# Kernel optimization log

Hardware: AMD Instinct MI355X
Metric: run time of the kernel (lower is better)

Reference implementation:

```python
import jax, jax.numpy as jnp
import numpy as np

N, IN_DIM, H, D = 4096, 512, 8, 64
NEG = -1e9  # additive mask value for non-edges


def setup_inputs() -> dict:
    key = jax.random.key(0)
    k1, k2, k3, k4, k5, k6 = jax.random.split(key, 6)
    data = jax.random.normal(k1, (N, IN_DIM), dtype=jnp.float32)
    r = jax.random.uniform(k2, (N, N), dtype=jnp.float32)
    connectivity = jnp.where(r < 0.05, 0.0, NEG).astype(jnp.float32)
    # xavier-uniform-ish init for params
    lim_w = float(np.sqrt(6.0 / (IN_DIM + H * D)))
    W = jax.random.uniform(k3, (H * D, IN_DIM), jnp.float32, -lim_w, lim_w)
    b = jnp.zeros((H * D,), jnp.float32)
    lim_p = float(np.sqrt(6.0 / (H * D + 1)))
    src_proj = jax.random.uniform(k4, (1, H, D), jnp.float32, -lim_p, lim_p)
    trg_proj = jax.random.uniform(k5, (1, H, D), jnp.float32, -lim_p, lim_p)
    return {"data": data, "connectivity": connectivity, "W": W, "b": b,
            "src_proj": src_proj, "trg_proj": trg_proj}


def reference(data, connectivity, W, b, src_proj, trg_proj):
    # dropout is identity in eval mode (reference is deterministic)
    data1 = (data @ W.T + b).reshape(N, H, D)          # (N,H,D)
    src = jnp.einsum('nhd,xhd->nh', data1, src_proj)   # (N,H)
    trg = jnp.einsum('nhd,xhd->nh', data1, trg_proj)   # (N,H)
    # scores: (H,N,1) + (H,1,N) broadcast outer-sum
    e = src.T[:, :, None] + trg.T[:, None, :]          # (H,N,N)
    e = jnp.where(e >= 0, e, 0.01 * e)                 # LeakyReLU(0.01)
    e = e + connectivity[None, :, :]                   # additive mask
    scores = jax.nn.softmax(e, axis=-1)                # (H,N,N)
    # bmm over heads: (H,N,N) x (H,N,D) -> (H,N,D)
    out = jnp.einsum('hnm,hmd->hnd', scores, data1.transpose(1, 0, 2))
    out = out.transpose(1, 0, 2).reshape(N, H * D)     # concat=True
    return out
```

## Files before the change

### kernel.cpp

```cpp
#include <hip/hip_runtime.h>
#include <hip/hip_bf16.h>

#define NN 4096
#define IN_DIM 512
#define NH 8
#define DD 64
#define HD 512
#define QCAP 128
#define RCAP 448


typedef __attribute__((ext_vector_type(8))) short short8;
typedef __attribute__((ext_vector_type(4))) float f32x4;
typedef __attribute__((ext_vector_type(2))) float f32x2;

static __device__ __forceinline__ unsigned short f2bf(float x) {
    __hip_bfloat16 h = __float2bfloat16(x);
    return *reinterpret_cast<unsigned short*>(&h);
}

__global__ __launch_bounds__(256) void k_cast2(const float* __restrict__ inA,
                                               unsigned short* __restrict__ outA,
                                               int n4A,
                                               const float* __restrict__ inB,
                                               unsigned short* __restrict__ outB,
                                               int n4B) {
    int t = blockIdx.x * 256 + threadIdx.x;
    const float* in;
    unsigned short* out;
    if (t < n4A) {
        in = inA; out = outA;
    } else {
        t -= n4A;
        if (t >= n4B) return;
        in = inB; out = outB;
    }
    float4 v = ((const float4*)in)[t];
    ushort4 o;
    o.x = f2bf(v.x); o.y = f2bf(v.y); o.z = f2bf(v.z); o.w = f2bf(v.w);
    ((ushort4*)out)[t] = o;
}

__global__ __launch_bounds__(256) void k_gemm_fused(const unsigned short* __restrict__ Ab,
                                                    const unsigned short* __restrict__ Wb,
                                                    const float* __restrict__ bias,
                                                    const float* __restrict__ sp,
                                                    const float* __restrict__ tp,
                                                    unsigned short* __restrict__ Cb,
                                                    float* __restrict__ src,
                                                    float* __restrict__ trg) {
    const int lane = threadIdx.x & 63;
    const int w = threadIdx.x >> 6;
    const int col = lane & 15;
    const int quad = lane >> 4;
    const int koff = quad * 8;
    const int h = blockIdx.x;
    const int m0 = h * 64;
    const int n0 = blockIdx.y * 64;

    const short8* ap  = (const short8*)(Ab + (size_t)(n0 + w * 16 + col) * IN_DIM + koff);
    const short8* bp0 = (const short8*)(Wb + (size_t)(m0 +  0 + col) * IN_DIM + koff);
    const short8* bp1 = (const short8*)(Wb + (size_t)(m0 + 16 + col) * IN_DIM + koff);
    const short8* bp2 = (const short8*)(Wb + (size_t)(m0 + 32 + col) * IN_DIM + koff);
    const short8* bp3 = (const short8*)(Wb + (size_t)(m0 + 48 + col) * IN_DIM + koff);

    f32x4 acc0 = {0.f, 0.f, 0.f, 0.f}, acc1 = acc0, acc2 = acc0, acc3 = acc0;

#pragma unroll 4
    for (int ks = 0; ks < 16; ks++) {
        short8 a  = ap[ks * 4];
        short8 b0 = bp0[ks * 4];
        short8 b1 = bp1[ks * 4];
        short8 b2 = bp2[ks * 4];
        short8 b3 = bp3[ks * 4];
        acc0 = __builtin_amdgcn_mfma_f32_16x16x32_bf16(a, b0, acc0, 0, 0, 0);
        acc1 = __builtin_amdgcn_mfma_f32_16x16x32_bf16(a, b1, acc1, 0, 0, 0);
        acc2 = __builtin_amdgcn_mfma_f32_16x16x32_bf16(a, b2, acc2, 0, 0, 0);
        acc3 = __builtin_amdgcn_mfma_f32_16x16x32_bf16(a, b3, acc3, 0, 0, 0);
    }

    const int rbase = n0 + w * 16 + quad * 4;
    f32x4 accs[4] = {acc0, acc1, acc2, acc3};
    float ps[4] = {0.f, 0.f, 0.f, 0.f};
    float pt[4] = {0.f, 0.f, 0.f, 0.f};
#pragma unroll
    for (int mt = 0; mt < 4; mt++) {
        const int m = m0 + mt * 16 + col;
        const float bv  = bias[m];
        const float spv = sp[m];
        const float tpv = tp[m];
#pragma unroll
        for (int r = 0; r < 4; r++) {
            float v = accs[mt][r] + bv;
            Cb[(size_t)(rbase + r) * HD + m] = f2bf(v);
            ps[r] += v * spv;
            pt[r] += v * tpv;
        }
    }
#pragma unroll
    for (int off = 1; off <= 8; off <<= 1) {
#pragma unroll
        for (int r = 0; r < 4; r++) {
            ps[r] += __shfl_xor(ps[r], off, 64);
            pt[r] += __shfl_xor(pt[r], off, 64);
        }
    }
    if (col < 4)
        src[(rbase + col) * 8 + h] = ps[col];
    else if (col < 8)
        trg[(rbase + col - 4) * 8 + h] = pt[col - 4];
}

__global__ __launch_bounds__(256) void k_rowattn(const float* __restrict__ conn,
                                                 const float* __restrict__ src,
                                                 const float* __restrict__ trg,
                                                 const unsigned short* __restrict__ d1b,
                                                 float* __restrict__ out) {
    __shared__ unsigned short seg[4][QCAP];
    __shared__ unsigned short elist[RCAP + 8];
    __shared__ int wcnt[4];
    __shared__ float cbuf[3][64][9];
    const int w = threadIdx.x >> 6, lane = threadIdx.x & 63;
    const int i = blockIdx.x;
    const int h = lane >> 3, d8 = lane & 7;

    const float* crow = conn + (size_t)i * NN + w * 1024;
    int cnt = 0;
#pragma unroll
    for (int c0 = 0; c0 < 1024; c0 += 256) {
        float4 c = *(const float4*)(crow + c0 + lane * 4);
        float cv[4] = {c.x, c.y, c.z, c.w};
#pragma unroll
        for (int q = 0; q < 4; q++) {
            bool edge = (cv[q] == 0.0f);
            unsigned long long mask = __ballot(edge);
            int pre = __popcll(mask & ((1ull << lane) - 1ull));
            int pos = cnt + pre;
            if (edge && pos < QCAP)
                seg[w][pos] = (unsigned short)(w * 1024 + c0 + lane * 4 + q);
            cnt += __popcll(mask);
        }
    }
    if (cnt > QCAP) cnt = QCAP;
    if (lane == 0) wcnt[w] = cnt;
    __syncthreads();

    const int c0n = wcnt[0], c1n = wcnt[1], c2n = wcnt[2], c3n = wcnt[3];
    int tot = c0n + c1n + c2n + c3n;
    if (tot > RCAP) tot = RCAP;
    const int base = (w == 0) ? 0 : (w == 1) ? c0n
                   : (w == 2) ? c0n + c1n : c0n + c1n + c2n;
    for (int k = lane; k < cnt && base + k < RCAP; k += 64)
        elist[base + k] = seg[w][k];
    __syncthreads();
    if (threadIdx.x < 4)
        elist[tot + threadIdx.x] = (tot > 0) ? elist[tot - 1] : (unsigned short)0;
    __syncthreads();

    const float sh = src[i * 8 + h];
    const unsigned voffB = (unsigned)(h * 64 + d8 * 8) * 2u;
    const unsigned toffB = (unsigned)h << 2;
    const unsigned char* vb = (const unsigned char*)d1b;
    const unsigned char* tb = (const unsigned char*)trg;
    const int kbeg = (tot * w) >> 2;
    const int kend = (tot * (w + 1)) >> 2;

    f32x2 a01 = {0.f, 0.f}, a23 = a01, a45 = a01, a67 = a01;
    float lsum = 0.f;
    if (kend > kbeg) {
        unsigned j0 = elist[kbeg];
        unsigned j1 = elist[kbeg + 1];
        unsigned j2 = elist[kbeg + 2];
        float t0 = *(const float*)(tb + (j0 << 5) + toffB);
        float t1 = *(const float*)(tb + (j1 << 5) + toffB);
        uint4 U0 = *(const uint4*)(vb + (j0 << 10) + voffB);
        uint4 U1 = *(const uint4*)(vb + (j1 << 10) + voffB);
#pragma unroll 3
        for (int k = kbeg; k < kend; k++) {
            unsigned j3 = elist[k + 3];
            float t2 = *(const float*)(tb + (j2 << 5) + toffB);
            uint4 U2 = *(const uint4*)(vb + (j2 << 10) + voffB);
            float e = sh + t0;
            e = fmaxf(e, 0.01f * e);
            float p = __expf(e);
            lsum += p;
            f32x2 p2 = {p, p};
            f32x2 v01 = {__uint_as_float(U0.x << 16), __uint_as_float(U0.x & 0xffff0000u)};
            f32x2 v23 = {__uint_as_float(U0.y << 16), __uint_as_float(U0.y & 0xffff0000u)};
            f32x2 v45 = {__uint_as_float(U0.z << 16), __uint_as_float(U0.z & 0xffff0000u)};
            f32x2 v67 = {__uint_as_float(U0.w << 16), __uint_as_float(U0.w & 0xffff0000u)};
            a01 += p2 * v01;
            a23 += p2 * v23;
            a45 += p2 * v45;
            a67 += p2 * v67;
            t0 = t1; t1 = t2;
            U0 = U1; U1 = U2;
            j2 = j3;
        }
    }

    float acc[8] = {a01.x, a01.y, a23.x, a23.y, a45.x, a45.y, a67.x, a67.y};
    if (w > 0) {
#pragma unroll
        for (int r = 0; r < 8; r++) cbuf[w - 1][lane][r] = acc[r];
        cbuf[w - 1][lane][8] = lsum;
    }
    __syncthreads();
    if (w == 0) {
#pragma unroll
        for (int wv = 0; wv < 3; wv++) {
#pragma unroll
            for (int r = 0; r < 8; r++) acc[r] += cbuf[wv][lane][r];
            lsum += cbuf[wv][lane][8];
        }
        float inv = (lsum > 0.f) ? (1.f / lsum) : 0.f;
        float* op = out + (size_t)i * HD + h * 64 + d8 * 8;
        *(float4*)op = make_float4(acc[0] * inv, acc[1] * inv, acc[2] * inv, acc[3] * inv);
        *(float4*)(op + 4) = make_float4(acc[4] * inv, acc[5] * inv, acc[6] * inv, acc[7] * inv);
    }
}

extern "C" void kernel_launch(void* const* d_in, const int* in_sizes, int n_in,
                              void* d_out, int out_size, void* d_ws, size_t ws_size,
                              hipStream_t stream) {
    const float* data = (const float*)d_in[0];
    const float* conn = (const float*)d_in[1];
    const float* W    = (const float*)d_in[2];
    const float* bias = (const float*)d_in[3];
    const float* sp   = (const float*)d_in[4];
    const float* tp   = (const float*)d_in[5];
    float* out = (float*)d_out;

    unsigned short* d1b = (unsigned short*)d_ws;
    unsigned short* Ab  = d1b + (size_t)NN * HD;
    unsigned short* Wb  = Ab + (size_t)NN * IN_DIM;
    float* src  = (float*)(Wb + (size_t)HD * IN_DIM);
    float* trg  = src + NN * NH;

    const int n4A = NN * IN_DIM / 4;
    const int n4B = HD * IN_DIM / 4;
    k_cast2<<<dim3((n4A + n4B + 255) / 256), 256, 0, stream>>>(data, Ab, n4A, W, Wb, n4B);
    k_gemm_fused<<<dim3(NH, NN / 64), 256, 0, stream>>>(Ab, Wb, bias, sp, tp, d1b, src, trg);
    k_rowattn<<<dim3(NN), 256, 0, stream>>>(conn, src, trg, d1b, out);
}
```

Before: 166.2 us.

## Split each wave into two half-waves processing alternate edges with 16 elements per lane

The row-attention gather loop now has each 64-lane wave work as two 32-lane halves. Each half takes every other edge in the wave's slice, and each lane loads 32 bytes (16 bf16 values) per edge instead of 16. The two halves' partial sums are combined with a cross-half shuffle before the existing cross-wave LDS reduction. This doubles the number of independent edge gathers in flight per wave and halves the loop trip count, in exchange for more accumulator registers and some wasted work on odd edge counts.

```diff
diff --git a/kernel.cpp b/kernel.cpp
--- a/kernel.cpp
+++ b/kernel.cpp
@@ -119,10 +119,9 @@
     __shared__ unsigned short seg[4][QCAP];
     __shared__ unsigned short elist[RCAP + 8];
     __shared__ int wcnt[4];
-    __shared__ float cbuf[3][64][9];
+    __shared__ float cbuf[3][32][17];
     const int w = threadIdx.x >> 6, lane = threadIdx.x & 63;
     const int i = blockIdx.x;
-    const int h = lane >> 3, d8 = lane & 7;
 
     const float* crow = conn + (size_t)i * NN + w * 1024;
     int cnt = 0;
@@ -153,70 +152,95 @@
     for (int k = lane; k < cnt && base + k < RCAP; k += 64)
         elist[base + k] = seg[w][k];
     __syncthreads();
-    if (threadIdx.x < 4)
+    if (threadIdx.x < 8)
         elist[tot + threadIdx.x] = (tot > 0) ? elist[tot - 1] : (unsigned short)0;
     __syncthreads();
 
+    const int e = lane >> 5;
+    const int l32 = lane & 31;
+    const int h = l32 >> 2;
+    const int d4 = l32 & 3;
     const float sh = src[i * 8 + h];
-    const unsigned voffB = (unsigned)(h * 64 + d8 * 8) * 2u;
-    const unsigned toffB = (unsigned)h << 2;
+    const unsigned voffB = (unsigned)(h * 128 + d4 * 32);
     const unsigned char* vb = (const unsigned char*)d1b;
-    const unsigned char* tb = (const unsigned char*)trg;
     const int kbeg = (tot * w) >> 2;
     const int kend = (tot * (w + 1)) >> 2;
-
-    f32x2 a01 = {0.f, 0.f}, a23 = a01, a45 = a01, a67 = a01;
+    const int np = (kend - kbeg + 1) >> 1;
+
+    f32x2 a0 = {0.f, 0.f}, a1 = a0, a2 = a0, a3 = a0,
+          a4 = a0, a5 = a0, a6 = a0, a7 = a0;
     float lsum = 0.f;
-    if (kend > kbeg) {
-        unsigned j0 = elist[kbeg];
-        unsigned j1 = elist[kbeg + 1];
-        unsigned j2 = elist[kbeg + 2];
-        float t0 = *(const float*)(tb + (j0 << 5) + toffB);
-        float t1 = *(const float*)(tb + (j1 << 5) + toffB);
-        uint4 U0 = *(const uint4*)(vb + (j0 << 10) + voffB);
-        uint4 U1 = *(const uint4*)(vb + (j1 << 10) + voffB);
-#pragma unroll 3
-        for (int k = kbeg; k < kend; k++) {
-            unsigned j3 = elist[k + 3];
-            float t2 = *(const float*)(tb + (j2 << 5) + toffB);
-            uint4 U2 = *(const uint4*)(vb + (j2 << 10) + voffB);
-            float e = sh + t0;
-            e = fmaxf(e, 0.01f * e);
-            float p = __expf(e);
+    if (np > 0) {
+        int myk = kbeg + e;
+        unsigned j0 = elist[myk];
+        unsigned j1 = elist[myk + 2];
+        unsigned j2 = elist[myk + 4];
+        float t0 = trg[j0 * 8 + h];
+        float t1 = trg[j1 * 8 + h];
+        uint4 U0a = *(const uint4*)(vb + (j0 << 10) + voffB);
+        uint4 U0b = *(const uint4*)(vb + (j0 << 10) + voffB + 16);
+        uint4 U1a = *(const uint4*)(vb + (j1 << 10) + voffB);
+        uint4 U1b = *(const uint4*)(vb + (j1 << 10) + voffB + 16);
+#pragma unroll 2
+        for (int kp = 0; kp < np; kp++) {
+            unsigned j3 = elist[myk + 6];
+            float t2 = trg[j2 * 8 + h];
+            uint4 U2a = *(const uint4*)(vb + (j2 << 10) + voffB);
+            uint4 U2b = *(const uint4*)(vb + (j2 << 10) + voffB + 16);
+            float ev = sh + t0;
+            ev = fmaxf(ev, 0.01f * ev);
+            float p = (myk < kend) ? __expf(ev) : 0.f;
             lsum += p;
             f32x2 p2 = {p, p};
-            f32x2 v01 = {__uint_as_float(U0.x << 16), __uint_as_float(U0.x & 0xffff0000u)};
-            f32x2 v23 = {__uint_as_float(U0.y << 16), __uint_as_float(U0.y & 0xffff0000u)};
-            f32x2 v45 = {__uint_as_float(U0.z << 16), __uint_as_float(U0.z & 0xffff0000u)};
-            f32x2 v67 = {__uint_as_float(U0.w << 16), __uint_as_float(U0.w & 0xffff0000u)};
-            a01 += p2 * v01;
-            a23 += p2 * v23;
-            a45 += p2 * v45;
-            a67 += p2 * v67;
+            f32x2 v0 = {__uint_as_float(U0a.x << 16), __uint_as_float(U0a.x & 0xffff0000u)};
+            f32x2 v1 = {__uint_as_float(U0a.y << 16), __uint_as_float(U0a.y & 0xffff0000u)};
+            f32x2 v2 = {__uint_as_float(U0a.z << 16), __uint_as_float(U0a.z & 0xffff0000u)};
+            f32x2 v3 = {__uint_as_float(U0a.w << 16), __uint_as_float(U0a.w & 0xffff0000u)};
+            f32x2 v4 = {__uint_as_float(U0b.x << 16), __uint_as_float(U0b.x & 0xffff0000u)};
+            f32x2 v5 = {__uint_as_float(U0b.y << 16), __uint_as_float(U0b.y & 0xffff0000u)};
+            f32x2 v6 = {__uint_as_float(U0b.z << 16), __uint_as_float(U0b.z & 0xffff0000u)};
+            f32x2 v7 = {__uint_as_float(U0b.w << 16), __uint_as_float(U0b.w & 0xffff0000u)};
+            a0 += p2 * v0;
+            a1 += p2 * v1;
+            a2 += p2 * v2;
+            a3 += p2 * v3;
+            a4 += p2 * v4;
+            a5 += p2 * v5;
+            a6 += p2 * v6;
+            a7 += p2 * v7;
+            myk += 2;
             t0 = t1; t1 = t2;
-            U0 = U1; U1 = U2;
+            U0a = U1a; U0b = U1b;
+            U1a = U2a; U1b = U2b;
             j2 = j3;
         }
     }
 
-    float acc[8] = {a01.x, a01.y, a23.x, a23.y, a45.x, a45.y, a67.x, a67.y};
-    if (w > 0) {
-#pragma unroll
-        for (int r = 0; r < 8; r++) cbuf[w - 1][lane][r] = acc[r];
-        cbuf[w - 1][lane][8] = lsum;
-    }
-    __syncthreads();
-    if (w == 0) {
+    float acc[16] = {a0.x, a0.y, a1.x, a1.y, a2.x, a2.y, a3.x, a3.y,
+                     a4.x, a4.y, a5.x, a5.y, a6.x, a6.y, a7.x, a7.y};
+#pragma unroll
+    for (int r = 0; r < 16; r++) acc[r] += __shfl_xor(acc[r], 32, 64);
+    lsum += __shfl_xor(lsum, 32, 64);
+
+    if (w > 0 && e == 0) {
+#pragma unroll
+        for (int r = 0; r < 16; r++) cbuf[w - 1][l32][r] = acc[r];
+        cbuf[w - 1][l32][16] = lsum;
+    }
+    __syncthreads();
+    if (w == 0 && e == 0) {
 #pragma unroll
         for (int wv = 0; wv < 3; wv++) {
 #pragma unroll
-            for (int r = 0; r < 8; r++) acc[r] += cbuf[wv][lane][r];
-            lsum += cbuf[wv][lane][8];
+            for (int r = 0; r < 16; r++) acc[r] += cbuf[wv][l32][r];
+            lsum += cbuf[wv][l32][16];
         }
         float inv = (lsum > 0.f) ? (1.f / lsum) : 0.f;
-        float* op = out + (size_t)i * HD + h * 64 + d8 * 8;
-        *(float4*)op = make_float4(acc[0] * inv, acc[1] * inv, acc[2] * inv, acc[3] * inv);
-        *(float4*)(op + 4) = make_float4(acc[4] * inv, acc[5] * inv, acc[6] * inv, acc[7] * inv);
+        float* op = out + (size_t)i * HD + h * 64 + d4 * 16;
+#pragma unroll
+        for (int q = 0; q < 4; q++)
+            *(float4*)(op + q * 4) = make_float4(acc[q * 4 + 0] * inv, acc[q * 4 + 1] * inv,
+                                                 acc[q * 4 + 2] * inv, acc[q * 4 + 3] * inv);
     }
 }
 
```

Measured after the change: 169.9 us. 1.02x slower.
